# Performance work log

Measured on AMD Instinct MI355X. Metric: run time of the kernel, lower is better.

The kernel has to match this reference:

```python
import jax, jax.numpy as jnp
import numpy as np

N = 500          # max_neurons, all alive
INPUT_SIZE = 3072
FEAT_DIM = 64
OUT_SIZE = 10
BATCH = 8192
RADIUS = 20.0
VOL = 100.0      # cubic volume (100,100,100)
N_ITER = 3


def setup_inputs() -> dict:
    key = jax.random.key(0)
    k_x, k_pos, k_iw, k_f, k_ow = jax.random.split(key, 5)
    x = jax.random.normal(k_x, (BATCH, INPUT_SIZE), dtype=jnp.float32)
    # seed positions spread across the volume, roughly matching _init_seeds
    positions = jax.random.uniform(k_pos, (N, 3), dtype=jnp.float32) * 80.0 + 10.0
    input_weights = jax.random.normal(k_iw, (N, INPUT_SIZE), dtype=jnp.float32) * 0.02
    features = jax.random.normal(k_f, (N, FEAT_DIM), dtype=jnp.float32) * 0.1
    output_weights = jax.random.normal(k_ow, (N, OUT_SIZE), dtype=jnp.float32) * 0.02
    biases = jnp.zeros((N,), dtype=jnp.float32)
    return {"x": x, "positions": positions, "input_weights": input_weights,
            "features": features, "output_weights": output_weights, "biases": biases}


def reference(x, positions, input_weights, features, output_weights, biases):
    # clamp positions into the volume (per-axis, vol is cubic here)
    pos = jnp.clip(positions, 0.1, VOL - 0.1)  # [N,3]

    # pairwise distances (grad-safe sqrt at the zero diagonal)
    diff = pos[:, None, :] - pos[None, :, :]          # [N,N,3]
    sq = jnp.sum(diff * diff, axis=-1)                # [N,N]
    pos_mask = sq > 0.0
    dist = jnp.where(pos_mask, jnp.sqrt(jnp.where(pos_mask, sq, 1.0)), 0.0)

    conn_mask = (dist < RADIUS) & (dist > 0.0)
    attenuation = jnp.exp(-dist / RADIUS) * conn_mask.astype(dist.dtype)

    # feature similarity (F.normalize clamps the norm from below at eps)
    feat_norm = features / jnp.maximum(
        jnp.linalg.norm(features, axis=1, keepdims=True), 1e-6)
    feat_sim = jnp.clip(feat_norm @ feat_norm.T, -1.0, 1.0)  # [N,N]

    conn_w = attenuation * (0.5 + 0.5 * feat_sim)
    conn_w = conn_w / (jnp.sum(conn_w, axis=1, keepdims=True) + 1e-6)

    # input gating: neurons near x=0 receive input
    x_norm = pos[:, 0] / VOL                          # [N]
    input_weight = jnp.exp(-2.0 * x_norm)
    input_weight = input_weight / (jnp.sum(input_weight) + 1e-6)

    activations = x @ input_weights.T * input_weight + biases  # [B,N]

    # iterative message passing (fixed small iteration count)
    for _ in range(N_ITER):
        msg = activations @ conn_w.T                  # [B,N]
        activations = jnp.minimum(jax.nn.relu(activations + 0.5 * msg), 50.0)

    # output gating: neurons near x=VOL emit output
    output_weight = jnp.exp(2.0 * (x_norm - 1.0))
    output_weight = output_weight / (jnp.sum(output_weight) + 1e-6)

    return activations @ (output_weights * output_weight[:, None])  # [B,OUT]
```

## Files before the change

### kernel.cpp

```cpp
#include <hip/hip_runtime.h>
#include <stdint.h>

#define N_REAL 500
#define NPAD   512
#define K_IN   3072
#define NBATCH 8192
#define NOUT   10
#define RADIUS 20.0f
#define VOLF   100.0f

typedef __attribute__((ext_vector_type(8))) __bf16 bf16x8;
typedef __attribute__((ext_vector_type(4))) float  f32x4;
typedef __attribute__((ext_vector_type(4))) unsigned short us4;

__device__ __forceinline__ unsigned short f2bf(float f) {
    unsigned int u = __float_as_uint(f);
    u += 0x7FFFu + ((u >> 16) & 1u);
    return (unsigned short)(u >> 16);
}
__device__ __forceinline__ float bf2f(unsigned short h) {
    return __uint_as_float(((unsigned int)h) << 16);
}
__device__ __forceinline__ bf16x8 cvt8(float4 lo, float4 hi) {
    union { unsigned int u[4]; bf16x8 v; } x;
    asm("v_cvt_pk_bf16_f32 %0, %1, %2" : "=v"(x.u[0]) : "v"(lo.x), "v"(lo.y));
    asm("v_cvt_pk_bf16_f32 %0, %1, %2" : "=v"(x.u[1]) : "v"(lo.z), "v"(lo.w));
    asm("v_cvt_pk_bf16_f32 %0, %1, %2" : "=v"(x.u[2]) : "v"(hi.x), "v"(hi.y));
    asm("v_cvt_pk_bf16_f32 %0, %1, %2" : "=v"(x.u[3]) : "v"(hi.z), "v"(hi.w));
    return x.v;
}

#define GLOBAL_AS __attribute__((address_space(1)))
#define LDS_AS    __attribute__((address_space(3)))
__device__ __forceinline__ void glds16(const void* g, void* l) {
    __builtin_amdgcn_global_load_lds((const GLOBAL_AS void*)g, (LDS_AS void*)l, 16, 0, 0);
}

__global__ void prep1(const float* __restrict__ positions,
                      const float* __restrict__ features,
                      const float* __restrict__ out_w,
                      const float* __restrict__ biases,
                      float* __restrict__ feat_norm,
                      float* __restrict__ pos_c,
                      float* __restrict__ inw,
                      float* __restrict__ biasp,
                      float* __restrict__ wout)
{
    int n = threadIdx.x;
    float e_in = 0.f, e_out = 0.f;
    float px = 0.f, py = 0.f, pz = 0.f;
    if (n < N_REAL) {
        px = fminf(fmaxf(positions[n*3+0], 0.1f), VOLF - 0.1f);
        py = fminf(fmaxf(positions[n*3+1], 0.1f), VOLF - 0.1f);
        pz = fminf(fmaxf(positions[n*3+2], 0.1f), VOLF - 0.1f);
        float xn = px / VOLF;
        e_in  = expf(-2.f * xn);
        e_out = expf(2.f * (xn - 1.f));
        float ss = 0.f;
        for (int f = 0; f < 64; ++f) { float v = features[n*64+f]; ss += v*v; }
        float nm = fmaxf(sqrtf(ss), 1e-6f);
        for (int f = 0; f < 64; ++f) feat_norm[n*64+f] = features[n*64+f] / nm;
    } else {
        for (int f = 0; f < 64; ++f) feat_norm[n*64+f] = 0.f;
    }
    pos_c[n*4+0] = px; pos_c[n*4+1] = py; pos_c[n*4+2] = pz; pos_c[n*4+3] = 0.f;

    __shared__ float s_in[512], s_out[512];
    s_in[n] = e_in; s_out[n] = e_out;
    __syncthreads();
    for (int s = 256; s > 0; s >>= 1) {
        if (n < s) { s_in[n] += s_in[n+s]; s_out[n] += s_out[n+s]; }
        __syncthreads();
    }
    float sum_in  = s_in[0]  + 1e-6f;
    float sum_out = s_out[0] + 1e-6f;

    inw[n]   = (n < N_REAL) ? (e_in / sum_in) : 0.f;
    biasp[n] = (n < N_REAL) ? biases[n] : 0.f;
    float wo = (n < N_REAL) ? (e_out / sum_out) : 0.f;
    for (int o = 0; o < NOUT; ++o)
        wout[n*NOUT + o] = (n < N_REAL) ? out_w[n*NOUT + o] * wo : 0.f;
}

__global__ void prep2(const float* __restrict__ pos_c,
                      const float* __restrict__ feat_norm,
                      unsigned short* __restrict__ conn_w)
{
    int i = blockIdx.x;
    int t = threadIdx.x;
    __shared__ float fi[64];
    __shared__ float spos[4];
    __shared__ float red[128];
    if (t < 64) fi[t] = feat_norm[i*64 + t];
    if (t < 4)  spos[t] = pos_c[i*4 + t];
    __syncthreads();

    float w[4];
    float part = 0.f;
    for (int jj = 0; jj < 4; ++jj) {
        int j = t + jj*128;
        float val = 0.f;
        if (i < N_REAL && j < N_REAL) {
            float dx = spos[0] - pos_c[j*4+0];
            float dy = spos[1] - pos_c[j*4+1];
            float dz = spos[2] - pos_c[j*4+2];
            float sq = dx*dx + dy*dy + dz*dz;
            if (sq > 0.f) {
                float dist = sqrtf(sq);
                if (dist < RADIUS) {
                    float att = expf(-dist / RADIUS);
                    float sim = 0.f;
                    const float4* fj = (const float4*)(feat_norm + j*64);
                    const float4* fi4 = (const float4*)fi;
                    #pragma unroll
                    for (int f = 0; f < 16; ++f) {
                        float4 a = fi4[f]; float4 b = fj[f];
                        sim += a.x*b.x + a.y*b.y + a.z*b.z + a.w*b.w;
                    }
                    sim = fminf(fmaxf(sim, -1.f), 1.f);
                    val = att * (0.5f + 0.5f*sim);
                }
            }
        }
        w[jj] = val; part += val;
    }
    red[t] = part;
    __syncthreads();
    for (int s = 64; s > 0; s >>= 1) {
        if (t < s) red[t] += red[t+s];
        __syncthreads();
    }
    float inv = 1.f / (red[0] + 1e-6f);
    for (int jj = 0; jj < 4; ++jj)
        conn_w[(long)i*NPAD + t + jj*128] = f2bf(w[jj] * inv);
}

__global__ void cast_pad(const float* __restrict__ src, unsigned short* __restrict__ dst,
                         long total_q, long src_q)
{
    long i = (long)blockIdx.x * blockDim.x + threadIdx.x;
    long stride = (long)gridDim.x * blockDim.x;
    for (; i < total_q; i += stride) {
        us4 o;
        if (i < src_q) {
            float4 v = ((const float4*)src)[i];
            o[0] = f2bf(v.x); o[1] = f2bf(v.y); o[2] = f2bf(v.z); o[3] = f2bf(v.w);
        } else {
            o[0] = 0; o[1] = 0; o[2] = 0; o[3] = 0;
        }
        ((us4*)dst)[i] = o;
    }
}

__device__ __forceinline__ void block_map(int b, int& m0, int& n0) {
    int xcd = b & 7, loc = b >> 3;
    m0 = (xcd*16 + (loc >> 1)) * 64;
    n0 = (loc & 1) * 256;
}

template<int MODE>
__global__ __launch_bounds__(512)
void gemm_main(const float* __restrict__ Xf,
               const unsigned short* __restrict__ Abf,
               const unsigned short* __restrict__ B,
               unsigned short* __restrict__ Cbf,
               const unsigned short* __restrict__ actOld,
               const float* __restrict__ inw,
               const float* __restrict__ biasp,
               int K)
{
    constexpr int ABUF = (MODE == 0) ? 16384 : 8192;
    constexpr int BBUF = 32768;
    __shared__ __align__(16) char lds[3*ABUF + 3*BBUF];

    const int tid  = threadIdx.x;
    const int lane = tid & 63;
    const int wave = tid >> 6;
    int m0, n0; block_map(blockIdx.x, m0, n0);
    const int wm = (wave >> 2) * 32;
    const int wn = (wave & 3) * 64;

    f32x4 acc[2][4];
    #pragma unroll
    for (int i = 0; i < 2; ++i)
        #pragma unroll
        for (int j = 0; j < 4; ++j)
            acc[i][j] = (f32x4){0.f,0.f,0.f,0.f};

    const char* gB[4]; int lBo[4];
    #pragma unroll
    for (int s = 0; s < 4; ++s) {
        int o = tid*16 + s*8192;
        int row = o >> 7, d = o & 127;
        gB[s] = (const char*)B + (long)(n0 + row) * (K*2) + (d ^ ((row & 7) << 4));
        lBo[s] = o;
    }
    const char* gA[2]; int lAo[2];
    if (MODE == 0) {
        #pragma unroll
        for (int s = 0; s < 2; ++s) {
            int o = tid*16 + s*8192;
            int row = o >> 8, slot = (o >> 4) & 15;
            gA[s] = (const char*)Xf + (long)(m0 + row) * (K*4) + ((slot ^ (row & 15)) << 4);
            lAo[s] = o;
        }
    } else {
        int o = tid*16;
        int row = o >> 7, d = o & 127;
        gA[0] = (const char*)Abf + (long)(m0 + row) * (K*2) + (d ^ ((row & 7) << 4));
        lAo[0] = o;
        gA[1] = nullptr; lAo[1] = 0;
    }

    const int NT = K >> 6;

#define ISSUE_TILE(p)                                                          \
    do {                                                                       \
        if (MODE == 0) {                                                       \
            glds16(gA[0], lds + (p)*ABUF + lAo[0]); gA[0] += 256;              \
            glds16(gA[1], lds + (p)*ABUF + lAo[1]); gA[1] += 256;              \
        } else {                                                               \
            glds16(gA[0], lds + (p)*ABUF + lAo[0]); gA[0] += 128;              \
        }                                                                      \
        glds16(gB[0], lds + 3*ABUF + (p)*BBUF + lBo[0]); gB[0] += 128;         \
        glds16(gB[1], lds + 3*ABUF + (p)*BBUF + lBo[1]); gB[1] += 128;         \
        glds16(gB[2], lds + 3*ABUF + (p)*BBUF + lBo[2]); gB[2] += 128;         \
        glds16(gB[3], lds + 3*ABUF + (p)*BBUF + lBo[3]); gB[3] += 128;         \
    } while (0)

    ISSUE_TILE(0);
    ISSUE_TILE(1);

    int cur = 0;
    for (int t = 0; t < NT; ++t) {
        int p2 = cur + 2; if (p2 >= 3) p2 -= 3;
        if (t + 2 < NT) {
            ISSUE_TILE(p2);
            if (MODE == 0) asm volatile("s_waitcnt vmcnt(12)" ::: "memory");
            else           asm volatile("s_waitcnt vmcnt(10)" ::: "memory");
        } else if (t + 1 < NT) {
            if (MODE == 0) asm volatile("s_waitcnt vmcnt(6)" ::: "memory");
            else           asm volatile("s_waitcnt vmcnt(5)" ::: "memory");
        } else {
            asm volatile("s_waitcnt vmcnt(0)" ::: "memory");
        }
        __builtin_amdgcn_s_barrier();

        const char* Ab = lds + cur*ABUF;
        const char* Bb = lds + 3*ABUF + cur*BBUF;
        #pragma unroll
        for (int kk = 0; kk < 2; ++kk) {
            bf16x8 afr[2], bfr[4];
            if (MODE == 0) {
                #pragma unroll
                for (int i = 0; i < 2; ++i) {
                    int r = wm + i*16 + (lane & 15);
                    int s0 = kk*8 + (lane >> 4)*2;
                    float4 lo = *(const float4*)(Ab + r*256 + (((s0    ) ^ (r & 15)) << 4));
                    float4 hi = *(const float4*)(Ab + r*256 + (((s0 + 1) ^ (r & 15)) << 4));
                    afr[i] = cvt8(lo, hi);
                }
            } else {
                #pragma unroll
                for (int i = 0; i < 2; ++i) {
                    int r = wm + i*16 + (lane & 15);
                    afr[i] = *(const bf16x8*)(Ab + r*128 + ((kk*64 + (lane >> 4)*16) ^ ((r & 7) << 4)));
                }
            }
            #pragma unroll
            for (int j = 0; j < 4; ++j) {
                int r = wn + j*16 + (lane & 15);
                bfr[j] = *(const bf16x8*)(Bb + r*128 + ((kk*64 + (lane >> 4)*16) ^ ((r & 7) << 4)));
            }
            #pragma unroll
            for (int i = 0; i < 2; ++i)
                #pragma unroll
                for (int j = 0; j < 4; ++j)
                    acc[i][j] = __builtin_amdgcn_mfma_f32_16x16x32_bf16(afr[i], bfr[j], acc[i][j], 0, 0, 0);
        }
        __builtin_amdgcn_s_barrier();
        cur = (cur == 2) ? 0 : cur + 1;
    }
#undef ISSUE_TILE

    const int mbase = m0 + wm + (lane >> 4) * 4;
    const int nbase = n0 + wn + (lane & 15);
    #pragma unroll
    for (int j = 0; j < 4; ++j) {
        const int n = nbase + j*16;
        float win = 0.f, bia = 0.f;
        if (MODE == 0) { win = inw[n]; bia = biasp[n]; }
        #pragma unroll
        for (int i = 0; i < 2; ++i)
            #pragma unroll
            for (int r = 0; r < 4; ++r) {
                const long m = mbase + i*16 + r;
                float vv;
                if (MODE == 0) {
                    vv = acc[i][j][r] * win + bia;
                } else {
                    float old = bf2f(actOld[m*NPAD + n]);
                    vv = fminf(fmaxf(old + 0.5f * acc[i][j][r], 0.f), 50.f);
                }
                Cbf[m*NPAD + n] = f2bf(vv);
            }
    }
}

__global__ __launch_bounds__(256)
void out_gemm(const unsigned short* __restrict__ act,
              const float* __restrict__ wout,
              float* __restrict__ out)
{
    __shared__ float sw[NPAD * NOUT];
    const int tid = threadIdx.x;
    for (int i = tid; i < NPAD*NOUT; i += 256) sw[i] = wout[i];
    __syncthreads();

    const int lane = tid & 63;
    const int wv   = tid >> 6;
    const int row  = blockIdx.x * 4 + wv;

    const unsigned short* ap = act + (long)row * NPAD + lane * 8;
    us4 v0 = *(const us4*)(ap);
    us4 v1 = *(const us4*)(ap + 4);

    float p[NOUT];
    #pragma unroll
    for (int o = 0; o < NOUT; ++o) p[o] = 0.f;

    const int nb = lane * 8;
    #pragma unroll
    for (int e = 0; e < 8; ++e) {
        float a = bf2f(e < 4 ? v0[e] : v1[e-4]);
        const float* wr = &sw[(nb + e) * NOUT];
        #pragma unroll
        for (int o = 0; o < NOUT; ++o) p[o] += a * wr[o];
    }
    #pragma unroll
    for (int o = 0; o < NOUT; ++o) {
        float s = p[o];
        for (int d = 32; d > 0; d >>= 1) s += __shfl_down(s, d);
        if (lane == 0) out[(long)row * NOUT + o] = s;
    }
}

extern "C" void kernel_launch(void* const* d_in, const int* in_sizes, int n_in,
                              void* d_out, int out_size, void* d_ws, size_t ws_size,
                              hipStream_t stream)
{
    const float* x        = (const float*)d_in[0];
    const float* pos      = (const float*)d_in[1];
    const float* in_w     = (const float*)d_in[2];
    const float* feats    = (const float*)d_in[3];
    const float* out_w    = (const float*)d_in[4];
    const float* biases   = (const float*)d_in[5];
    float* out = (float*)d_out;

    char* ws = (char*)d_ws;
    unsigned short* iw_bf  = (unsigned short*)(ws);
    unsigned short* connw  = (unsigned short*)(ws + 3145728);
    unsigned short* act_a  = (unsigned short*)(ws + 3670016);
    unsigned short* act_b  = (unsigned short*)(ws + 12058624);
    float* feat_norm = (float*)(ws + 20447232);
    float* pos_c     = (float*)(ws + 20578304);
    float* inw       = (float*)(ws + 20586496);
    float* biasp     = (float*)(ws + 20588544);
    float* wout      = (float*)(ws + 20590592);

    prep1<<<1, 512, 0, stream>>>(pos, feats, out_w, biases, feat_norm, pos_c, inw, biasp, wout);
    prep2<<<512, 128, 0, stream>>>(pos_c, feat_norm, connw);
    cast_pad<<<512, 256, 0, stream>>>(in_w, iw_bf, 393216L, 384000L);

    gemm_main<0><<<256, 512, 0, stream>>>(x, nullptr, iw_bf, act_a, nullptr, inw, biasp, K_IN);
    gemm_main<1><<<256, 512, 0, stream>>>(nullptr, act_a, connw, act_b, act_a, nullptr, nullptr, NPAD);
    gemm_main<1><<<256, 512, 0, stream>>>(nullptr, act_b, connw, act_a, act_b, nullptr, nullptr, NPAD);
    gemm_main<1><<<256, 512, 0, stream>>>(nullptr, act_a, connw, act_b, act_a, nullptr, nullptr, NPAD);

    out_gemm<<<NBATCH/4, 256, 0, stream>>>(act_b, wout, out);
}
```

Baseline: 132.8 us.

## Load A operand directly to registers and shrink tiles to 64x128 blocks

The templated GEMM is split into two kernels. Each now loads the activation/input A operand straight from global memory into registers, double-buffered, so the A tile no longer goes through LDS. The B tile is 64x128 with a 4-deep LDS ring, blocks are 256 threads with launch bounds allowing 2 blocks per CU, and the grid doubles to 512 blocks. This cuts LDS footprint and LDS traffic for A and aims to raise occupancy. The cost is that A rows are read by every N-block with no LDS sharing, which increases global/L2 traffic, and the hand-tuned vmcnt counts must match the new load counts.

```diff
diff --git a/kernel.cpp b/kernel.cpp
--- a/kernel.cpp
+++ b/kernel.cpp
@@ -154,31 +154,26 @@
 
 __device__ __forceinline__ void block_map(int b, int& m0, int& n0) {
     int xcd = b & 7, loc = b >> 3;
-    m0 = (xcd*16 + (loc >> 1)) * 64;
-    n0 = (loc & 1) * 256;
-}
-
-template<int MODE>
-__global__ __launch_bounds__(512)
-void gemm_main(const float* __restrict__ Xf,
-               const unsigned short* __restrict__ Abf,
+    m0 = (xcd*16 + (loc >> 2)) * 64;
+    n0 = (loc & 3) * 128;
+}
+
+__global__ __launch_bounds__(256, 2)
+void gemm1_dir(const float* __restrict__ X,
                const unsigned short* __restrict__ B,
                unsigned short* __restrict__ Cbf,
-               const unsigned short* __restrict__ actOld,
                const float* __restrict__ inw,
-               const float* __restrict__ biasp,
-               int K)
-{
-    constexpr int ABUF = (MODE == 0) ? 16384 : 8192;
-    constexpr int BBUF = 32768;
-    __shared__ __align__(16) char lds[3*ABUF + 3*BBUF];
+               const float* __restrict__ biasp)
+{
+    constexpr int BBUF = 16384;
+    __shared__ __align__(16) char lds[4*BBUF];
 
     const int tid  = threadIdx.x;
     const int lane = tid & 63;
     const int wave = tid >> 6;
     int m0, n0; block_map(blockIdx.x, m0, n0);
-    const int wm = (wave >> 2) * 32;
-    const int wn = (wave & 3) * 64;
+    const int wm = (wave >> 1) * 32;
+    const int wn = (wave & 1) * 64;
 
     f32x4 acc[2][4];
     #pragma unroll
@@ -190,118 +185,205 @@
     const char* gB[4]; int lBo[4];
     #pragma unroll
     for (int s = 0; s < 4; ++s) {
-        int o = tid*16 + s*8192;
+        int o = tid*16 + s*4096;
         int row = o >> 7, d = o & 127;
-        gB[s] = (const char*)B + (long)(n0 + row) * (K*2) + (d ^ ((row & 7) << 4));
+        gB[s] = (const char*)B + (long)(n0 + row) * (K_IN*2) + (d ^ ((row & 7) << 4));
         lBo[s] = o;
     }
-    const char* gA[2]; int lAo[2];
-    if (MODE == 0) {
-        #pragma unroll
-        for (int s = 0; s < 2; ++s) {
-            int o = tid*16 + s*8192;
-            int row = o >> 8, slot = (o >> 4) & 15;
-            gA[s] = (const char*)Xf + (long)(m0 + row) * (K*4) + ((slot ^ (row & 15)) << 4);
-            lAo[s] = o;
-        }
-    } else {
-        int o = tid*16;
-        int row = o >> 7, d = o & 127;
-        gA[0] = (const char*)Abf + (long)(m0 + row) * (K*2) + (d ^ ((row & 7) << 4));
-        lAo[0] = o;
-        gA[1] = nullptr; lAo[1] = 0;
-    }
-
-    const int NT = K >> 6;
-
-#define ISSUE_TILE(p)                                                          \
-    do {                                                                       \
-        if (MODE == 0) {                                                       \
-            glds16(gA[0], lds + (p)*ABUF + lAo[0]); gA[0] += 256;              \
-            glds16(gA[1], lds + (p)*ABUF + lAo[1]); gA[1] += 256;              \
-        } else {                                                               \
-            glds16(gA[0], lds + (p)*ABUF + lAo[0]); gA[0] += 128;              \
-        }                                                                      \
-        glds16(gB[0], lds + 3*ABUF + (p)*BBUF + lBo[0]); gB[0] += 128;         \
-        glds16(gB[1], lds + 3*ABUF + (p)*BBUF + lBo[1]); gB[1] += 128;         \
-        glds16(gB[2], lds + 3*ABUF + (p)*BBUF + lBo[2]); gB[2] += 128;         \
-        glds16(gB[3], lds + 3*ABUF + (p)*BBUF + lBo[3]); gB[3] += 128;         \
-    } while (0)
-
-    ISSUE_TILE(0);
-    ISSUE_TILE(1);
-
-    int cur = 0;
-    for (int t = 0; t < NT; ++t) {
-        int p2 = cur + 2; if (p2 >= 3) p2 -= 3;
-        if (t + 2 < NT) {
-            ISSUE_TILE(p2);
-            if (MODE == 0) asm volatile("s_waitcnt vmcnt(12)" ::: "memory");
-            else           asm volatile("s_waitcnt vmcnt(10)" ::: "memory");
-        } else if (t + 1 < NT) {
-            if (MODE == 0) asm volatile("s_waitcnt vmcnt(6)" ::: "memory");
-            else           asm volatile("s_waitcnt vmcnt(5)" ::: "memory");
-        } else {
-            asm volatile("s_waitcnt vmcnt(0)" ::: "memory");
-        }
-        __builtin_amdgcn_s_barrier();
-
-        const char* Ab = lds + cur*ABUF;
-        const char* Bb = lds + 3*ABUF + cur*BBUF;
-        #pragma unroll
-        for (int kk = 0; kk < 2; ++kk) {
-            bf16x8 afr[2], bfr[4];
-            if (MODE == 0) {
-                #pragma unroll
-                for (int i = 0; i < 2; ++i) {
-                    int r = wm + i*16 + (lane & 15);
-                    int s0 = kk*8 + (lane >> 4)*2;
-                    float4 lo = *(const float4*)(Ab + r*256 + (((s0    ) ^ (r & 15)) << 4));
-                    float4 hi = *(const float4*)(Ab + r*256 + (((s0 + 1) ^ (r & 15)) << 4));
-                    afr[i] = cvt8(lo, hi);
-                }
-            } else {
-                #pragma unroll
-                for (int i = 0; i < 2; ++i) {
-                    int r = wm + i*16 + (lane & 15);
-                    afr[i] = *(const bf16x8*)(Ab + r*128 + ((kk*64 + (lane >> 4)*16) ^ ((r & 7) << 4)));
-                }
-            }
-            #pragma unroll
-            for (int j = 0; j < 4; ++j) {
-                int r = wn + j*16 + (lane & 15);
-                bfr[j] = *(const bf16x8*)(Bb + r*128 + ((kk*64 + (lane >> 4)*16) ^ ((r & 7) << 4)));
-            }
-            #pragma unroll
-            for (int i = 0; i < 2; ++i)
-                #pragma unroll
-                for (int j = 0; j < 4; ++j)
-                    acc[i][j] = __builtin_amdgcn_mfma_f32_16x16x32_bf16(afr[i], bfr[j], acc[i][j], 0, 0, 0);
-        }
-        __builtin_amdgcn_s_barrier();
-        cur = (cur == 2) ? 0 : cur + 1;
-    }
-#undef ISSUE_TILE
+    const float* pA0 = X + (long)(m0 + wm +      (lane & 15)) * K_IN + ((lane >> 4) * 8);
+    const float* pA1 = X + (long)(m0 + wm + 16 + (lane & 15)) * K_IN + ((lane >> 4) * 8);
+
+    float4 va0[4], va1[4], vb0[4], vb1[4];
+
+#define LOADA1(d0, d1, koff) do {                                        \
+    _Pragma("unroll")                                                    \
+    for (int f = 0; f < 4; ++f) {                                        \
+        const float* p = ((f >> 1) ? pA1 : pA0) + (koff) + (f & 1)*32;   \
+        d0[f] = *(const float4*)(p);                                     \
+        d1[f] = *(const float4*)(p + 4);                                 \
+    } } while (0)
+
+#define ISSUEB1(bi) do {                                                 \
+    _Pragma("unroll")                                                    \
+    for (int s = 0; s < 4; ++s) {                                        \
+        glds16(gB[s], lds + (bi)*BBUF + lBo[s]); gB[s] += 128;           \
+    } } while (0)
+
+    const int NT = K_IN >> 6;
+
+    LOADA1(va0, va1, 0);
+    __builtin_amdgcn_sched_barrier(0);
+    ISSUEB1(0);
+    ISSUEB1(1);
+
+#define STEP1(t, AC0, AC1, AN0, AN1) do {                                        \
+    const int bufc = (t) & 3;                                                    \
+    if ((t) + 1 < NT) {                                                          \
+        LOADA1(AN0, AN1, ((t)+1)*64);                                            \
+        __builtin_amdgcn_sched_barrier(0);                                       \
+    }                                                                            \
+    if ((t) + 2 < NT) {                                                          \
+        ISSUEB1(((t)+2) & 3);                                                    \
+        asm volatile("s_waitcnt vmcnt(16)" ::: "memory");                        \
+    } else if ((t) + 1 < NT) {                                                   \
+        asm volatile("s_waitcnt vmcnt(12)" ::: "memory");                        \
+    } else {                                                                     \
+        asm volatile("s_waitcnt vmcnt(0)" ::: "memory");                         \
+    }                                                                            \
+    __builtin_amdgcn_s_barrier();                                                \
+    const char* Bb = lds + bufc*BBUF;                                            \
+    _Pragma("unroll")                                                            \
+    for (int kk = 0; kk < 2; ++kk) {                                             \
+        bf16x8 afr[2], bfr[4];                                                   \
+        afr[0] = cvt8(AC0[kk],     AC1[kk]);                                     \
+        afr[1] = cvt8(AC0[2 + kk], AC1[2 + kk]);                                 \
+        const int cb = kk*64 + (lane >> 4) * 16;                                 \
+        _Pragma("unroll")                                                        \
+        for (int j = 0; j < 4; ++j) {                                            \
+            int r = wn + j*16 + (lane & 15);                                     \
+            bfr[j] = *(const bf16x8*)(Bb + r*128 + (cb ^ ((r & 7) << 4)));       \
+        }                                                                        \
+        _Pragma("unroll")                                                        \
+        for (int i = 0; i < 2; ++i)                                              \
+            _Pragma("unroll")                                                    \
+            for (int j = 0; j < 4; ++j)                                          \
+                acc[i][j] = __builtin_amdgcn_mfma_f32_16x16x32_bf16(             \
+                                afr[i], bfr[j], acc[i][j], 0, 0, 0);             \
+    } } while (0)
+
+    for (int t = 0; t < NT; t += 2) {
+        STEP1(t,     va0, va1, vb0, vb1);
+        STEP1(t + 1, vb0, vb1, va0, va1);
+    }
+#undef STEP1
+#undef LOADA1
+#undef ISSUEB1
 
     const int mbase = m0 + wm + (lane >> 4) * 4;
     const int nbase = n0 + wn + (lane & 15);
     #pragma unroll
     for (int j = 0; j < 4; ++j) {
         const int n = nbase + j*16;
-        float win = 0.f, bia = 0.f;
-        if (MODE == 0) { win = inw[n]; bia = biasp[n]; }
+        const float win = inw[n], bia = biasp[n];
         #pragma unroll
         for (int i = 0; i < 2; ++i)
             #pragma unroll
             for (int r = 0; r < 4; ++r) {
                 const long m = mbase + i*16 + r;
-                float vv;
-                if (MODE == 0) {
-                    vv = acc[i][j][r] * win + bia;
-                } else {
-                    float old = bf2f(actOld[m*NPAD + n]);
-                    vv = fminf(fmaxf(old + 0.5f * acc[i][j][r], 0.f), 50.f);
-                }
+                Cbf[m*NPAD + n] = f2bf(acc[i][j][r] * win + bia);
+            }
+    }
+}
+
+__global__ __launch_bounds__(256, 2)
+void gemm2_dir(const unsigned short* __restrict__ A,
+               const unsigned short* __restrict__ B,
+               unsigned short* __restrict__ Cbf,
+               const unsigned short* __restrict__ actOld)
+{
+    constexpr int BBUF = 16384;
+    __shared__ __align__(16) char lds[4*BBUF];
+
+    const int tid  = threadIdx.x;
+    const int lane = tid & 63;
+    const int wave = tid >> 6;
+    int m0, n0; block_map(blockIdx.x, m0, n0);
+    const int wm = (wave >> 1) * 32;
+    const int wn = (wave & 1) * 64;
+
+    f32x4 acc[2][4];
+    #pragma unroll
+    for (int i = 0; i < 2; ++i)
+        #pragma unroll
+        for (int j = 0; j < 4; ++j)
+            acc[i][j] = (f32x4){0.f,0.f,0.f,0.f};
+
+    const char* gB[4]; int lBo[4];
+    #pragma unroll
+    for (int s = 0; s < 4; ++s) {
+        int o = tid*16 + s*4096;
+        int row = o >> 7, d = o & 127;
+        gB[s] = (const char*)B + (long)(n0 + row) * (NPAD*2) + (d ^ ((row & 7) << 4));
+        lBo[s] = o;
+    }
+    const unsigned short* pA0 = A + (long)(m0 + wm +      (lane & 15)) * NPAD + ((lane >> 4) * 8);
+    const unsigned short* pA1 = A + (long)(m0 + wm + 16 + (lane & 15)) * NPAD + ((lane >> 4) * 8);
+
+    bf16x8 wa[4], wb[4];
+
+#define LOADA2(dst, koff) do {                                           \
+    _Pragma("unroll")                                                    \
+    for (int f = 0; f < 4; ++f) {                                        \
+        const unsigned short* p = ((f >> 1) ? pA1 : pA0) + (koff) + (f & 1)*32; \
+        dst[f] = *(const bf16x8*)(p);                                    \
+    } } while (0)
+
+#define ISSUEB2(bi) do {                                                 \
+    _Pragma("unroll")                                                    \
+    for (int s = 0; s < 4; ++s) {                                        \
+        glds16(gB[s], lds + (bi)*BBUF + lBo[s]); gB[s] += 128;           \
+    } } while (0)
+
+    const int NT = NPAD >> 6;
+
+    LOADA2(wa, 0);
+    __builtin_amdgcn_sched_barrier(0);
+    ISSUEB2(0);
+    ISSUEB2(1);
+
+#define STEP2(t, AC, AN) do {                                                    \
+    const int bufc = (t) & 3;                                                    \
+    if ((t) + 1 < NT) {                                                          \
+        LOADA2(AN, ((t)+1)*64);                                                  \
+        __builtin_amdgcn_sched_barrier(0);                                       \
+    }                                                                            \
+    if ((t) + 2 < NT) {                                                          \
+        ISSUEB2(((t)+2) & 3);                                                    \
+        asm volatile("s_waitcnt vmcnt(12)" ::: "memory");                        \
+    } else if ((t) + 1 < NT) {                                                   \
+        asm volatile("s_waitcnt vmcnt(8)" ::: "memory");                         \
+    } else {                                                                     \
+        asm volatile("s_waitcnt vmcnt(0)" ::: "memory");                         \
+    }                                                                            \
+    __builtin_amdgcn_s_barrier();                                                \
+    const char* Bb = lds + bufc*BBUF;                                            \
+    _Pragma("unroll")                                                            \
+    for (int kk = 0; kk < 2; ++kk) {                                             \
+        bf16x8 bfr[4];                                                           \
+        const int cb = kk*64 + (lane >> 4) * 16;                                 \
+        _Pragma("unroll")                                                        \
+        for (int j = 0; j < 4; ++j) {                                            \
+            int r = wn + j*16 + (lane & 15);                                     \
+            bfr[j] = *(const bf16x8*)(Bb + r*128 + (cb ^ ((r & 7) << 4)));       \
+        }                                                                        \
+        _Pragma("unroll")                                                        \
+        for (int i = 0; i < 2; ++i)                                              \
+            _Pragma("unroll")                                                    \
+            for (int j = 0; j < 4; ++j)                                          \
+                acc[i][j] = __builtin_amdgcn_mfma_f32_16x16x32_bf16(             \
+                                AC[i*2 + kk], bfr[j], acc[i][j], 0, 0, 0);       \
+    } } while (0)
+
+    for (int t = 0; t < NT; t += 2) {
+        STEP2(t,     wa, wb);
+        STEP2(t + 1, wb, wa);
+    }
+#undef STEP2
+#undef LOADA2
+#undef ISSUEB2
+
+    const int mbase = m0 + wm + (lane >> 4) * 4;
+    const int nbase = n0 + wn + (lane & 15);
+    #pragma unroll
+    for (int j = 0; j < 4; ++j) {
+        const int n = nbase + j*16;
+        #pragma unroll
+        for (int i = 0; i < 2; ++i)
+            #pragma unroll
+            for (int r = 0; r < 4; ++r) {
+                const long m = mbase + i*16 + r;
+                float old = bf2f(actOld[m*NPAD + n]);
+                float vv = fminf(fmaxf(old + 0.5f * acc[i][j][r], 0.f), 50.f);
                 Cbf[m*NPAD + n] = f2bf(vv);
             }
     }
@@ -372,10 +454,10 @@
     prep2<<<512, 128, 0, stream>>>(pos_c, feat_norm, connw);
     cast_pad<<<512, 256, 0, stream>>>(in_w, iw_bf, 393216L, 384000L);
 
-    gemm_main<0><<<256, 512, 0, stream>>>(x, nullptr, iw_bf, act_a, nullptr, inw, biasp, K_IN);
-    gemm_main<1><<<256, 512, 0, stream>>>(nullptr, act_a, connw, act_b, act_a, nullptr, nullptr, NPAD);
-    gemm_main<1><<<256, 512, 0, stream>>>(nullptr, act_b, connw, act_a, act_b, nullptr, nullptr, NPAD);
-    gemm_main<1><<<256, 512, 0, stream>>>(nullptr, act_a, connw, act_b, act_a, nullptr, nullptr, NPAD);
+    gemm1_dir<<<512, 256, 0, stream>>>(x, iw_bf, act_a, inw, biasp);
+    gemm2_dir<<<512, 256, 0, stream>>>(act_a, connw, act_b, act_a);
+    gemm2_dir<<<512, 256, 0, stream>>>(act_b, connw, act_a, act_b);
+    gemm2_dir<<<512, 256, 0, stream>>>(act_a, connw, act_b, act_a);
 
     out_gemm<<<NBATCH/4, 256, 0, stream>>>(act_b, wout, out);
 }
```

Measured after the change: 191.6 us. 1.44x slower.
